# Performance work log

Hardware: AMD Instinct MI355X
Metric: run time of the kernel (lower is better)

The kernel has to match this reference:

```python
import jax, jax.numpy as jnp
import numpy as np


def setup_inputs() -> dict:
    key = jax.random.key(0)
    ks = jax.random.split(key, 7)
    B, T, Fin, H, O = 32, 2048, 256, 256, 256
    s = 1.0 / np.sqrt(H)
    return {
        "x":   jax.random.normal(ks[0], (B, T, Fin), dtype=jnp.float32),
        "h0":  jax.random.normal(ks[1], (B, H), dtype=jnp.float32),
        "Wxh": jax.random.normal(ks[2], (H, Fin), dtype=jnp.float32) * s,
        "bxh": jax.random.normal(ks[3], (H,), dtype=jnp.float32) * s,
        "Whh": jax.random.normal(ks[4], (H, H), dtype=jnp.float32) * s,
        "Why": jax.random.normal(ks[5], (O, H), dtype=jnp.float32) * s,
        "by":  jax.random.normal(ks[6], (O,), dtype=jnp.float32) * s,
    }


def reference(x, h0, Wxh, bxh, Whh, Why, by):
    # Batch the input projection across all T as one GEMM: (B,T,Fin)x(Fin,H)
    xh = jnp.einsum('btf,hf->bth', x, Wxh) + bxh  # (B,T,H)

    def step(h, xh_t):
        h = jnp.tanh(xh_t + h @ Whh.T)  # (B,H)
        return h, h

    # scan over time (axis 0 after transpose)
    h_final, hs = jax.lax.scan(step, h0, jnp.swapaxes(xh, 0, 1))  # hs: (T,B,H)
    hs = jnp.swapaxes(hs, 0, 1)  # (B,T,H)
    # Batch the output projection across all T as one GEMM
    y = jnp.einsum('bth,oh->bto', hs, Why) + by  # (B,T,O)
    return (y, h_final)
```

## Files before the change

### kernel.cpp

```cpp
#include <hip/hip_runtime.h>
#include <hip/hip_bf16.h>
#include <hip/hip_fp16.h>


typedef _Float16 f16x8 __attribute__((ext_vector_type(8)));
typedef float    f32x4 __attribute__((ext_vector_type(4)));

#define MFMA16 __builtin_amdgcn_mfma_f32_16x16x32_f16

__device__ __forceinline__ f16x8 cvt8(const float* __restrict__ p) {
    float4 u = *(const float4*)p;
    float4 v = *(const float4*)(p + 4);
    f16x8 r;
    r[0] = (_Float16)u.x; r[1] = (_Float16)u.y; r[2] = (_Float16)u.z; r[3] = (_Float16)u.w;
    r[4] = (_Float16)v.x; r[5] = (_Float16)v.y; r[6] = (_Float16)v.z; r[7] = (_Float16)v.w;
    return r;
}

template<bool AF16>
__global__ __launch_bounds__(256, 2) void gemm_nt_256(
    const void* __restrict__ Av, const float* __restrict__ W,
    const float* __restrict__ bias, float* __restrict__ C) {
    const int tid = threadIdx.x;
    const int l  = tid & 63;
    const int w  = tid >> 6;
    const int lr = l & 15;
    const int lg = l >> 4;
    const long m0 = (long)blockIdx.x * 64;
    const int  n0 = w * 64;

    f32x4 acc[4][4] = {};

    #pragma unroll
    for (int k = 0; k < 8; ++k) {
        const int kc = k * 32 + lg * 8;
        f16x8 a[4], bf[4];
        #pragma unroll
        for (int mt = 0; mt < 4; ++mt) {
            const long row = m0 + mt * 16 + lr;
            if constexpr (AF16)
                a[mt] = *(const f16x8*)((const _Float16*)Av + row * 256 + kc);
            else
                a[mt] = cvt8((const float*)Av + row * 256 + kc);
        }
        #pragma unroll
        for (int nt = 0; nt < 4; ++nt)
            bf[nt] = cvt8(W + (long)(n0 + nt * 16 + lr) * 256 + kc);
        #pragma unroll
        for (int mt = 0; mt < 4; ++mt)
            #pragma unroll
            for (int nt = 0; nt < 4; ++nt)
                acc[mt][nt] = MFMA16(a[mt], bf[nt], acc[mt][nt], 0, 0, 0);
    }

    #pragma unroll
    for (int mt = 0; mt < 4; ++mt)
        #pragma unroll
        for (int nt = 0; nt < 4; ++nt) {
            const int col = n0 + nt * 16 + lr;
            const float bv = bias[col];
            #pragma unroll
            for (int d = 0; d < 4; ++d) {
                const long row = m0 + mt * 16 + lg * 4 + d;
                C[row * 256 + col] = acc[mt][nt][d] + bv;
            }
        }
}

__global__ __launch_bounds__(512, 1) void rnn_scan(
    const float* __restrict__ xh, const float* __restrict__ h0,
    const float* __restrict__ Whh, _Float16* __restrict__ hs,
    float* __restrict__ hfin) {
    const int b   = blockIdx.x;
    const int tid = threadIdx.x;
    const int l   = tid & 63;
    const int w   = tid >> 6;
    const int lr  = l & 15;
    const int lg  = l >> 4;
    const int n0  = w * 32;

    __shared__ _Float16 hbuf[2][256];

    f16x8 wb[2][8];
    #pragma unroll
    for (int nt = 0; nt < 2; ++nt)
        #pragma unroll
        for (int k = 0; k < 8; ++k)
            wb[nt][k] = cvt8(Whh + (long)(n0 + nt * 16 + lr) * 256 + k * 32 + lg * 8);

    if (tid < 256) hbuf[0][tid] = (_Float16)h0[b * 256 + tid];
    __syncthreads();

    const int cl = n0 + (l & 31);
    const float* xp = xh + (long)b * 2048 * 256 + cl;
    _Float16*    hp = hs + (long)b * 2048 * 256 + cl;

    float xcur[4], xnext[4];
    #pragma unroll
    for (int j = 0; j < 4; ++j) xcur[j] = xp[(long)j * 256];

    for (int tb = 0; tb < 2048; tb += 4) {
        #pragma unroll
        for (int j = 0; j < 4; ++j) {
            long tn = tb + 4 + j; if (tn > 2047) tn = 2047;
            xnext[j] = xp[tn * 256];
        }

        #pragma unroll
        for (int j = 0; j < 4; ++j) {
            const f16x8* hc = (const f16x8*)hbuf[j & 1];
            f16x8 af[8];
            #pragma unroll
            for (int k = 0; k < 8; ++k) af[k] = hc[k * 4 + lg];
            __builtin_amdgcn_sched_barrier(0);

            const f32x4 zero = {0.f, 0.f, 0.f, 0.f};
            f32x4 accA[2], accB[2];
            #pragma unroll
            for (int nt = 0; nt < 2; ++nt) {
                accA[nt] = MFMA16(af[0], wb[nt][0], zero, 0, 0, 0);
                accB[nt] = MFMA16(af[4], wb[nt][4], zero, 0, 0, 0);
            }
            #pragma unroll
            for (int k = 1; k < 4; ++k)
                #pragma unroll
                for (int nt = 0; nt < 2; ++nt) {
                    accA[nt] = MFMA16(af[k],     wb[nt][k],     accA[nt], 0, 0, 0);
                    accB[nt] = MFMA16(af[k + 4], wb[nt][k + 4], accB[nt], 0, 0, 0);
                }

            const float s0 = accA[0][0] + accB[0][0];
            const float s1 = accA[1][0] + accB[1][0];
            const float s  = ((l & 16) ? s1 : s0) + xcur[j];
            const float e  = __expf(2.0f * s);
            const float v  = 1.0f - 2.0f * __builtin_amdgcn_rcpf(e + 1.0f);
            const _Float16 hv = (_Float16)v;

            if (l < 32) {
                hbuf[(j & 1) ^ 1][cl] = hv;
                hp[(long)(tb + j) * 256] = hv;
            }

            asm volatile("s_waitcnt lgkmcnt(0)" ::: "memory");
            __builtin_amdgcn_s_barrier();
            asm volatile("" ::: "memory");
        }

        #pragma unroll
        for (int j = 0; j < 4; ++j) xcur[j] = xnext[j];
    }

    if (tid < 256) hfin[b * 256 + tid] = (float)hbuf[0][tid];
}

extern "C" void kernel_launch(void* const* d_in, const int* in_sizes, int n_in,
                              void* d_out, int out_size, void* d_ws, size_t ws_size,
                              hipStream_t stream) {
    const float* x   = (const float*)d_in[0];
    const float* h0  = (const float*)d_in[1];
    const float* Wxh = (const float*)d_in[2];
    const float* bxh = (const float*)d_in[3];
    const float* Whh = (const float*)d_in[4];
    const float* Why = (const float*)d_in[5];
    const float* by  = (const float*)d_in[6];

    float* y    = (float*)d_out;
    float* hfin = y + (long)65536 * 256;
    float* xh   = y;
    _Float16* hs = (_Float16*)d_ws;

    gemm_nt_256<false><<<1024, 256, 0, stream>>>(x, Wxh, bxh, xh);
    rnn_scan<<<32, 512, 0, stream>>>(xh, h0, Whh, hs, hfin);
    gemm_nt_256<true><<<1024, 256, 0, stream>>>(hs, Why, by, y);
}
```

Before: 935.2 us.

## Register-resident weight GEMM tiles, fp16 xh intermediate, and MFMA priority in scan

The GEMM kernel now uses 512 threads per block, each wave keeping its 32-column slice of the weight matrix in registers as fp16 and streaming 128 rows of A through it. This removes the repeated per-k reloads and conversions of W. The input projection is now written as fp16 into the back half of the output buffer, which halves the bytes written by the first GEMM and read by the scan. The scan also drops the sched_barrier and raises wave priority around its MFMA chain. The costs are lower precision for xh and a changed instruction schedule.

Result: no change. 920.2 us (-1.6%).

```diff
diff --git a/kernel.cpp b/kernel.cpp
--- a/kernel.cpp
+++ b/kernel.cpp
@@ -1,5 +1,4 @@
 #include <hip/hip_runtime.h>
-#include <hip/hip_bf16.h>
 #include <hip/hip_fp16.h>
 
 
@@ -17,58 +16,58 @@
     return r;
 }
 
-template<bool AF16>
-__global__ __launch_bounds__(256, 2) void gemm_nt_256(
+template<bool AF16, bool OF16>
+__global__ __launch_bounds__(512, 2) void gemm_nt_512(
     const void* __restrict__ Av, const float* __restrict__ W,
-    const float* __restrict__ bias, float* __restrict__ C) {
+    const float* __restrict__ bias, void* __restrict__ Cv) {
     const int tid = threadIdx.x;
     const int l  = tid & 63;
     const int w  = tid >> 6;
     const int lr = l & 15;
     const int lg = l >> 4;
-    const long m0 = (long)blockIdx.x * 64;
-    const int  n0 = w * 64;
+    const long m0 = (long)blockIdx.x * 128;
+    const int  n0 = w * 32;
 
-    f32x4 acc[4][4] = {};
+    f16x8 wg[2][8];
+    #pragma unroll
+    for (int nt = 0; nt < 2; ++nt)
+        #pragma unroll
+        for (int k = 0; k < 8; ++k)
+            wg[nt][k] = cvt8(W + (long)(n0 + nt * 16 + lr) * 256 + k * 32 + lg * 8);
 
-    #pragma unroll
-    for (int k = 0; k < 8; ++k) {
-        const int kc = k * 32 + lg * 8;
-        f16x8 a[4], bf[4];
+    const float bv0 = bias[n0 + lr];
+    const float bv1 = bias[n0 + 16 + lr];
+
+    #pragma unroll 2
+    for (int mt = 0; mt < 8; ++mt) {
+        const long r0 = m0 + mt * 16 + lr;
+        f32x4 ac[2] = {{0.f,0.f,0.f,0.f},{0.f,0.f,0.f,0.f}};
         #pragma unroll
-        for (int mt = 0; mt < 4; ++mt) {
-            const long row = m0 + mt * 16 + lr;
-            if constexpr (AF16)
-                a[mt] = *(const f16x8*)((const _Float16*)Av + row * 256 + kc);
-            else
-                a[mt] = cvt8((const float*)Av + row * 256 + kc);
+        for (int k = 0; k < 8; ++k) {
+            const int kc = k * 32 + lg * 8;
+            f16x8 a;
+            if constexpr (AF16) a = *(const f16x8*)((const _Float16*)Av + r0 * 256 + kc);
+            else                a = cvt8((const float*)Av + r0 * 256 + kc);
+            ac[0] = MFMA16(a, wg[0][k], ac[0], 0, 0, 0);
+            ac[1] = MFMA16(a, wg[1][k], ac[1], 0, 0, 0);
         }
         #pragma unroll
-        for (int nt = 0; nt < 4; ++nt)
-            bf[nt] = cvt8(W + (long)(n0 + nt * 16 + lr) * 256 + kc);
-        #pragma unroll
-        for (int mt = 0; mt < 4; ++mt)
-            #pragma unroll
-            for (int nt = 0; nt < 4; ++nt)
-                acc[mt][nt] = MFMA16(a[mt], bf[nt], acc[mt][nt], 0, 0, 0);
-    }
-
-    #pragma unroll
-    for (int mt = 0; mt < 4; ++mt)
-        #pragma unroll
-        for (int nt = 0; nt < 4; ++nt) {
+        for (int nt = 0; nt < 2; ++nt) {
             const int col = n0 + nt * 16 + lr;
-            const float bv = bias[col];
+            const float bv = nt ? bv1 : bv0;
             #pragma unroll
             for (int d = 0; d < 4; ++d) {
                 const long row = m0 + mt * 16 + lg * 4 + d;
-                C[row * 256 + col] = acc[mt][nt][d] + bv;
+                const float v = ac[nt][d] + bv;
+                if constexpr (OF16) ((_Float16*)Cv)[row * 256 + col] = (_Float16)v;
+                else                ((float*)Cv)[row * 256 + col] = v;
             }
         }
+    }
 }
 
 __global__ __launch_bounds__(512, 1) void rnn_scan(
-    const float* __restrict__ xh, const float* __restrict__ h0,
+    const _Float16* __restrict__ xh, const float* __restrict__ h0,
     const float* __restrict__ Whh, _Float16* __restrict__ hs,
     float* __restrict__ hfin) {
     const int b   = blockIdx.x;
@@ -92,18 +91,18 @@
     __syncthreads();
 
     const int cl = n0 + (l & 31);
-    const float* xp = xh + (long)b * 2048 * 256 + cl;
-    _Float16*    hp = hs + (long)b * 2048 * 256 + cl;
+    const _Float16* xp = xh + (long)b * 2048 * 256 + cl;
+    _Float16*       hp = hs + (long)b * 2048 * 256 + cl;
 
     float xcur[4], xnext[4];
     #pragma unroll
-    for (int j = 0; j < 4; ++j) xcur[j] = xp[(long)j * 256];
+    for (int j = 0; j < 4; ++j) xcur[j] = (float)xp[(long)j * 256];
 
     for (int tb = 0; tb < 2048; tb += 4) {
         #pragma unroll
         for (int j = 0; j < 4; ++j) {
             long tn = tb + 4 + j; if (tn > 2047) tn = 2047;
-            xnext[j] = xp[tn * 256];
+            xnext[j] = (float)xp[tn * 256];
         }
 
         #pragma unroll
@@ -112,8 +111,8 @@
             f16x8 af[8];
             #pragma unroll
             for (int k = 0; k < 8; ++k) af[k] = hc[k * 4 + lg];
-            __builtin_amdgcn_sched_barrier(0);
 
+            __builtin_amdgcn_s_setprio(1);
             const f32x4 zero = {0.f, 0.f, 0.f, 0.f};
             f32x4 accA[2], accB[2];
             #pragma unroll
@@ -128,6 +127,7 @@
                     accA[nt] = MFMA16(af[k],     wb[nt][k],     accA[nt], 0, 0, 0);
                     accB[nt] = MFMA16(af[k + 4], wb[nt][k + 4], accB[nt], 0, 0, 0);
                 }
+            __builtin_amdgcn_s_setprio(0);
 
             const float s0 = accA[0][0] + accB[0][0];
             const float s1 = accA[1][0] + accB[1][0];
@@ -166,10 +166,10 @@
 
     float* y    = (float*)d_out;
     float* hfin = y + (long)65536 * 256;
-    float* xh   = y;
-    _Float16* hs = (_Float16*)d_ws;
+    _Float16* xhf = (_Float16*)(y + (long)32768 * 256);
+    _Float16* hs  = (_Float16*)d_ws;
 
-    gemm_nt_256<false><<<1024, 256, 0, stream>>>(x, Wxh, bxh, xh);
-    rnn_scan<<<32, 512, 0, stream>>>(xh, h0, Whh, hs, hfin);
-    gemm_nt_256<true><<<1024, 256, 0, stream>>>(hs, Why, by, y);
+    gemm_nt_512<false, true ><<<512, 512, 0, stream>>>(x, Wxh, bxh, xhf);
+    rnn_scan<<<32, 512, 0, stream>>>(xhf, h0, Whh, hs, hfin);
+    gemm_nt_512<true,  false><<<512, 512, 0, stream>>>(hs, Why, by, y);
 }
```
